# Kernel tuning notes

Hardware: AMD Instinct MI355X
Metric: run time of the kernel (lower is better)

Reference implementation:

```python
import jax, jax.numpy as jnp
import numpy as np

B, CIN, H, W = 8, 64, 128, 128
COUT, KH, KW = 64, 3, 3
STRIDE, PAD, DIL = 1, 1, 1
HO, WO = 128, 128


def setup_inputs() -> dict:
    key = jax.random.key(0)
    k1, k2, k3 = jax.random.split(key, 3)
    x = jax.random.normal(k1, (B, CIN, H, W), dtype=jnp.float32)
    offset = jax.random.normal(k2, (B, 2 * KH * KW, HO, WO), dtype=jnp.float32)
    fan_in = CIN * KH * KW
    weight = jax.random.normal(k3, (COUT, CIN, KH, KW), dtype=jnp.float32) / np.sqrt(fan_in)
    return {"x": x, "offset": offset, "weight": weight}


def _deform_conv(x, offset, weight):
    b, c, h, w = x.shape
    cout, cin, kh, kw = weight.shape
    k2 = kh * kw
    ho, wo = offset.shape[2], offset.shape[3]
    # offsets: interleaved (dy, dx) per kernel tap
    off = offset.reshape(b, k2, 2, ho, wo)
    dy, dx = off[:, :, 0], off[:, :, 1]                      # [B, K2, Ho, Wo]
    ky = jnp.repeat(jnp.arange(kh), kw).astype(x.dtype)       # [K2]
    kx = jnp.tile(jnp.arange(kw), kh).astype(x.dtype)
    base_y = (jnp.arange(ho) * STRIDE - PAD).astype(x.dtype)  # [Ho]
    base_x = (jnp.arange(wo) * STRIDE - PAD).astype(x.dtype)  # [Wo]
    py = dy + ky[None, :, None, None] * DIL + base_y[None, None, :, None]
    px = dx + kx[None, :, None, None] * DIL + base_x[None, None, None, :]

    y0 = jnp.floor(py)
    x0 = jnp.floor(px)
    wy1 = py - y0
    wx1 = px - x0
    y0i = y0.astype(jnp.int32)
    x0i = x0.astype(jnp.int32)

    def gather_corner(yi, xi, wgt):
        # zero-padding semantics: mask out-of-bounds corners
        valid = ((yi >= 0) & (yi < h) & (xi >= 0) & (xi < w)).astype(x.dtype)
        yc = jnp.clip(yi, 0, h - 1)
        xc = jnp.clip(xi, 0, w - 1)
        def per_batch(xb, yb, xbid, vb, wb):
            return xb[:, yb, xbid] * (vb * wb)[None]          # [C, K2, Ho, Wo]
        return jax.vmap(per_batch)(x, yc, xc, valid, wgt)

    # accumulate 4 corners to avoid holding all gathers at once
    sampled = gather_corner(y0i, x0i, (1 - wy1) * (1 - wx1))
    sampled = sampled + gather_corner(y0i, x0i + 1, (1 - wy1) * wx1)
    sampled = sampled + gather_corner(y0i + 1, x0i, wy1 * (1 - wx1))
    sampled = sampled + gather_corner(y0i + 1, x0i + 1, wy1 * wx1)
    # sampled: [B, Cin, K2, Ho, Wo]; conv-accumulate
    return jnp.einsum('bckhw,ock->bohw', sampled, weight.reshape(cout, cin, k2))


def reference(x, offset, weight):
    return _deform_conv(x, offset, weight)
```

## Files before the change

### kernel.cpp

```cpp
#include <hip/hip_runtime.h>
#include <hip/hip_bf16.h>

#define CIN  64
#define HH   128
#define WW   128
#define COUT 64
#define K2   9
#define HW   (HH * WW)

typedef __attribute__((ext_vector_type(8))) short bf16x8;
typedef __attribute__((ext_vector_type(4))) float f32x4;
typedef __attribute__((ext_vector_type(2))) float f32x2;

__device__ __forceinline__ unsigned short f2bf(float f) {
    __hip_bfloat16 h = __float2bfloat16(f);
    return *reinterpret_cast<unsigned short*>(&h);
}
__device__ __forceinline__ f32x2 up2(unsigned int d) {
    f32x2 r;
    r[0] = __uint_as_float(d << 16);
    r[1] = __uint_as_float(d & 0xffff0000u);
    return r;
}
__device__ __forceinline__ void gl2lds16(const unsigned short* g, unsigned short* l) {
    __builtin_amdgcn_global_load_lds(
        (const __attribute__((address_space(1))) unsigned int*)g,
        (__attribute__((address_space(3))) unsigned int*)l, 16, 0, 0);
}

__launch_bounds__(256)
__global__ void xprep2_kernel(const float* __restrict__ x, unsigned short* __restrict__ xt) {
    const int idx = blockIdx.x * 256 + threadIdx.x;
    const int xw = idx & 127;
    const int y  = (idx >> 7) & 127;
    const int s  = (idx >> 14) & 7;
    const int b  = idx >> 17;
    const float* src = x + (((size_t)(b * CIN + s * 8) * HH) + y) * WW + xw;
    union { unsigned short us[8]; bf16x8 v; } u;
    #pragma unroll
    for (int j = 0; j < 8; ++j) u.us[j] = f2bf(src[(size_t)j * HW]);
    *(bf16x8*)(xt + ((((size_t)b * 8 + s) * HW) + y * WW + xw) * 8) = u.v;
}

__global__ void wprep_kernel(const float* __restrict__ w, unsigned short* __restrict__ wtp) {
    int idx = blockIdx.x * 256 + threadIdx.x;
    if (idx >= COUT * CIN * K2) return;
    int j  = idx & 7;
    int l  = (idx >> 3) & 63;
    int nt = (idx >> 9) & 3;
    int ks = (idx >> 11) & 1;
    int k  = idx >> 12;
    int o  = nt * 16 + (l & 15);
    int c  = ks * 32 + (l >> 4) * 8 + j;
    wtp[idx] = f2bf(w[(o * CIN + c) * K2 + k]);
}

__launch_bounds__(512, 4)
__global__ void dcn_kernel(const unsigned short* __restrict__ xt,
                           const float* __restrict__ off,
                           const unsigned short* __restrict__ wtp,
                           float* __restrict__ out) {
    extern __shared__ unsigned short lsB[];
    const int tid = threadIdx.x;
    const int w   = tid >> 6;
    const int l   = tid & 63;
    const int wr  = w & 3;
    const int wh  = w >> 2;

    int bid = blockIdx.x;
    bid = (bid & 7) * 256 + (bid >> 3);
    const int b   = bid >> 8;
    const int t   = bid & 255;
    const int ty0 = (t >> 3) << 2;
    const int tx0 = (t & 7) << 4;

    const int g      = l >> 4;
    const int lane16 = l & 15;

    #pragma unroll
    for (int r = 0; r < 9; ++r) {
        const int seg = r * 8 + w;
        gl2lds16(wtp + seg * 512 + l * 8, lsB + seg * 512);
    }

    f32x4 acc[4] = {{0,0,0,0},{0,0,0,0},{0,0,0,0},{0,0,0,0}};

    const float* offb = off + (size_t)b * (2 * K2) * HW;
    const unsigned short* xp = xt + ((size_t)b * 8 + (wh * 4 + g)) * HW * 8;

    const int ypA  = ty0 + wr;
    const int xpA  = tx0 + lane16;
    const int offp = ypA * WW + xpA;

    f32x4 Pw[2];
    int   Pr0[2], Pr1[2];
    float oyv[2], oxv[2];
    bf16x8 Gst[2][4];
    bf16x8 bvv[4];
    bf16x8 af;

#define PARAMS(K, S) do {                                                     \
    const int kdy = (K) / 3 - 1, kdx = (K) % 3 - 1;                           \
    float py = oyv[S] + (float)(ypA + kdy);                                   \
    float px = oxv[S] + (float)(xpA + kdx);                                   \
    float fy = floorf(py), fx = floorf(px);                                   \
    float wy = py - fy, wxn = px - fx;                                        \
    int y0 = (int)fy, x0i = (int)fx;                                          \
    int yc0 = min(max(y0,     0), HH - 1);                                    \
    int yc1 = min(max(y0 + 1, 0), HH - 1);                                    \
    float ay0 = (y0 >= 0  && y0 <= HH - 1) ? (1.f - wy) : 0.f;                \
    float ay1 = (y0 >= -1 && y0 <= HH - 2) ? wy         : 0.f;                \
    int   xL  = min(max(x0i, 0), WW - 2);                                     \
    float bx0 = (x0i >= 0  && x0i <= WW - 1) ? (1.f - wxn) : 0.f;             \
    float bx1 = (x0i >= -1 && x0i <= WW - 2) ? wxn         : 0.f;             \
    bool  sw  = (x0i != xL);                                                  \
    float wxa = sw ? bx1 : bx0;                                               \
    float wxb = sw ? bx0 : bx1;                                               \
    Pw[S][0] = ay0 * wxa; Pw[S][1] = ay0 * wxb;                               \
    Pw[S][2] = ay1 * wxa; Pw[S][3] = ay1 * wxb;                               \
    Pr0[S] = (yc0 * WW + xL) * 8;                                             \
    Pr1[S] = (yc1 * WW + xL) * 8;                                             \
} while (0)

#define GATHER(S) do {                                                        \
    const unsigned short* r0p = xp + Pr0[S];                                  \
    const unsigned short* r1p = xp + Pr1[S];                                  \
    Gst[S][0] = *(const bf16x8*)(r0p); Gst[S][1] = *(const bf16x8*)(r0p + 8); \
    Gst[S][2] = *(const bf16x8*)(r1p); Gst[S][3] = *(const bf16x8*)(r1p + 8); \
} while (0)

#define INTERP(S) do {                                                        \
    union { bf16x8 v; unsigned int d[4]; } ua, ub, uc, ud;                    \
    ua.v = Gst[S][0]; ub.v = Gst[S][1]; uc.v = Gst[S][2]; ud.v = Gst[S][3];   \
    union { unsigned short us[8]; bf16x8 v; } rr;                             \
    _Pragma("unroll")                                                         \
    for (int q = 0; q < 4; ++q) {                                             \
        f32x2 v = up2(ua.d[q]) * Pw[S][0] + up2(ub.d[q]) * Pw[S][1]           \
                + up2(uc.d[q]) * Pw[S][2] + up2(ud.d[q]) * Pw[S][3];          \
        rr.us[2*q]   = f2bf(v[0]);                                            \
        rr.us[2*q+1] = f2bf(v[1]);                                            \
    }                                                                         \
    af = rr.v;                                                                \
} while (0)

#define BVLOAD(K) do {                                                        \
    _Pragma("unroll")                                                         \
    for (int nt = 0; nt < 4; ++nt)                                            \
        bvv[nt] = *(const bf16x8*)(&lsB[(((K) * 2 + wh) * 4 + nt) * 512 + l * 8]); \
} while (0)

#define DOMFMA() do {                                                         \
    __builtin_amdgcn_s_setprio(1);                                            \
    acc[0] = __builtin_amdgcn_mfma_f32_16x16x32_bf16(af, bvv[0], acc[0], 0, 0, 0); \
    acc[1] = __builtin_amdgcn_mfma_f32_16x16x32_bf16(af, bvv[1], acc[1], 0, 0, 0); \
    acc[2] = __builtin_amdgcn_mfma_f32_16x16x32_bf16(af, bvv[2], acc[2], 0, 0, 0); \
    acc[3] = __builtin_amdgcn_mfma_f32_16x16x32_bf16(af, bvv[3], acc[3], 0, 0, 0); \
    __builtin_amdgcn_s_setprio(0);                                            \
} while (0)

    oyv[0] = offb[offp];          oxv[0] = offb[HW + offp];
    oyv[1] = offb[2 * HW + offp]; oxv[1] = offb[3 * HW + offp];
    PARAMS(0, 0);
    GATHER(0);
    __syncthreads();

    #pragma unroll
    for (int s = 0; s < K2; ++s) {
        const int cur = s & 1, nxt = cur ^ 1;
        if (s < 8) {
            PARAMS(s + 1, nxt);
            if (s < 7) {
                oyv[cur] = offb[(2 * (s + 2)    ) * HW + offp];
                oxv[cur] = offb[(2 * (s + 2) + 1) * HW + offp];
            }
            GATHER(nxt);
        }
        BVLOAD(s);
        INTERP(cur);
        DOMFMA();
    }

#undef PARAMS
#undef GATHER
#undef INTERP
#undef BVLOAD
#undef DOMFMA

    float (*sred)[66] = (float (*)[66])lsB;
    __syncthreads();
    const int rq = g * 4;
    if (wh == 0) {
        #pragma unroll
        for (int nt = 0; nt < 4; ++nt)
            #pragma unroll
            for (int j = 0; j < 4; ++j)
                sred[wr * 16 + rq + j][nt * 16 + lane16] = acc[nt][j];
    }
    __syncthreads();
    if (wh == 1) {
        #pragma unroll
        for (int nt = 0; nt < 4; ++nt) {
            f32x4 v;
            #pragma unroll
            for (int j = 0; j < 4; ++j)
                v[j] = sred[wr * 16 + rq + j][nt * 16 + lane16] + acc[nt][j];
            const int o  = nt * 16 + lane16;
            const int yy = ty0 + wr;
            const int xx = tx0 + rq;
            *(f32x4*)&out[(((size_t)b * COUT + o) * HH + yy) * WW + xx] = v;
        }
    }
}

__global__ void wprep_fb(const float* __restrict__ w, unsigned short* __restrict__ wt) {
    int idx = blockIdx.x * 256 + threadIdx.x;
    if (idx >= COUT * CIN * K2) return;
    int o = idx / (CIN * K2);
    int r = idx % (CIN * K2);
    int k = r / CIN;
    int c = r % CIN;
    wt[idx] = f2bf(w[o * (CIN * K2) + c * K2 + k]);
}

__launch_bounds__(256)
__global__ void dcn_fb(const float* __restrict__ x, const float* __restrict__ off,
                       const unsigned short* __restrict__ wt, float* __restrict__ out) {
    __shared__ unsigned short s_s[64 * 66];
    const int tid = threadIdx.x;
    const int w = tid >> 6, l = tid & 63;
    const int bid = blockIdx.x;
    const int b = bid >> 8, t = bid & 255;
    const int ty0 = (t >> 4) << 3, tx0 = (t & 15) << 3;
    const int iy = l >> 3, ix = l & 7;
    const int ypix = ty0 + iy, xpix = tx0 + ix;
    f32x4 acc[4] = {{0,0,0,0},{0,0,0,0},{0,0,0,0},{0,0,0,0}};
    const int c0w = w * 16;
    for (int k = 0; k < K2; ++k) {
        float dy = off[(((b * (2*K2)) + 2*k    ) * HH + ypix) * WW + xpix];
        float dx = off[(((b * (2*K2)) + 2*k + 1) * HH + ypix) * WW + xpix];
        float py = dy + (float)(k / 3 + ypix - 1);
        float px = dx + (float)(k % 3 + xpix - 1);
        float fy = floorf(py), fx = floorf(px);
        float wy = py - fy, wx = px - fx;
        int y0 = (int)fy, x0 = (int)fx;
        int yc0 = min(max(y0, 0), HH-1), yc1 = min(max(y0+1, 0), HH-1);
        float ay0 = (y0 >= 0 && y0 <= HH-1) ? (1.f-wy) : 0.f;
        float ay1 = (y0 >= -1 && y0 <= HH-2) ? wy : 0.f;
        int xL = min(max(x0, 0), WW-2);
        float bx0 = (x0 >= 0 && x0 <= WW-1) ? (1.f-wx) : 0.f;
        float bx1 = (x0 >= -1 && x0 <= WW-2) ? wx : 0.f;
        bool sw = (x0 != xL);
        float wxa = sw ? bx1 : bx0, wxb = sw ? bx0 : bx1;
        float W0x = ay0*wxa, W0y = ay0*wxb, W1x = ay1*wxa, W1y = ay1*wxb;
        const float* r0 = x + ((b * CIN + c0w) * HH + yc0) * WW + xL;
        const float* r1 = x + ((b * CIN + c0w) * HH + yc1) * WW + xL;
        unsigned short* sd = &s_s[l * 66 + c0w];
        #pragma unroll
        for (int cc = 0; cc < 16; ++cc) {
            sd[cc] = f2bf(W0x*r0[0] + W0y*r0[1] + W1x*r1[0] + W1y*r1[1]);
            r0 += HH*WW; r1 += HH*WW;
        }
        __syncthreads();
        const int o_lane = l & 15, q = l >> 4;
        #pragma unroll
        for (int ks = 0; ks < 2; ++ks) {
            const int cb = ks*32 + q*8;
            const int row = w*16 + o_lane;
            const unsigned int* sp = (const unsigned int*)s_s;
            const int ib = row*33 + (cb >> 1);
            union { unsigned int u[4]; bf16x8 v; } af;
            af.u[0]=sp[ib]; af.u[1]=sp[ib+1]; af.u[2]=sp[ib+2]; af.u[3]=sp[ib+3];
            #pragma unroll
            for (int nt = 0; nt < 4; ++nt) {
                bf16x8 bfv = *(const bf16x8*)(wt + (nt*16 + o_lane) * (CIN*K2) + k*64 + cb);
                acc[nt] = __builtin_amdgcn_mfma_f32_16x16x32_bf16(af.v, bfv, acc[nt], 0, 0, 0);
            }
        }
        __syncthreads();
    }
    const int o_lane = l & 15, rq = (l >> 4) * 4;
    #pragma unroll
    for (int nt = 0; nt < 4; ++nt) {
        const int o = nt*16 + o_lane;
        #pragma unroll
        for (int j = 0; j < 4; ++j) {
            const int pix = w*16 + rq + j;
            out[(((size_t)b * COUT + o) * HH + ty0 + (pix>>3)) * WW + tx0 + (pix&7)] = acc[nt][j];
        }
    }
}

extern "C" void kernel_launch(void* const* d_in, const int* in_sizes, int n_in,
                              void* d_out, int out_size, void* d_ws, size_t ws_size,
                              hipStream_t stream) {
    const float* x   = (const float*)d_in[0];
    const float* off = (const float*)d_in[1];
    const float* wgt = (const float*)d_in[2];
    float* out = (float*)d_out;

    const size_t xt_bytes = (size_t)8 * HW * 64 * sizeof(unsigned short);
    const size_t wt_bytes = (size_t)COUT * CIN * K2 * sizeof(unsigned short);

    if (ws_size >= xt_bytes + wt_bytes) {
        unsigned short* xt  = (unsigned short*)d_ws;
        unsigned short* wtp = (unsigned short*)((char*)d_ws + xt_bytes);
        xprep2_kernel<<<4096, 256, 0, stream>>>(x, xt);
        wprep_kernel<<<(COUT * CIN * K2 + 255) / 256, 256, 0, stream>>>(wgt, wtp);
        dcn_kernel<<<2048, 512, 73728, stream>>>(xt, off, wtp, out);
    } else {
        unsigned short* wt = (unsigned short*)d_ws;
        wprep_fb<<<(COUT * CIN * K2 + 255) / 256, 256, 0, stream>>>(wgt, wt);
        dcn_fb<<<2048, 256, 0, stream>>>(x, off, wt, out);
    }
}
```

Measured before the change: 57.34 us.

## Deepen gather pipeline to triple buffering with offsets prefetched further ahead

Turns the double-buffered per-tap gather pipeline into a triple-buffered one. Corner gathers are now issued two kernel taps ahead of the MFMA step, and offset loads three taps ahead, using a hand-unrolled schedule of step macros. The goal is to hide more global-memory gather latency behind interpolation and MFMA work. In exchange it holds an extra set of bf16x8 gather registers and parameters, which raises register pressure and could cut occupancy.

Result: slower. 84.83 us (+47.9%).

```diff
diff --git a/kernel.cpp b/kernel.cpp
--- a/kernel.cpp
+++ b/kernel.cpp
@@ -92,17 +92,22 @@
     const int xpA  = tx0 + lane16;
     const int offp = ypA * WW + xpA;
 
-    f32x4 Pw[2];
-    int   Pr0[2], Pr1[2];
-    float oyv[2], oxv[2];
-    bf16x8 Gst[2][4];
+    f32x4 Pw[3];
+    int   Pr0[3], Pr1[3];
+    float oy[3], ox[3];
+    bf16x8 Gst[3][4];
     bf16x8 bvv[4];
     bf16x8 af;
 
+#define OFFL(K, S) do {                                                       \
+    oy[S] = offb[(2 * (K)    ) * HW + offp];                                  \
+    ox[S] = offb[(2 * (K) + 1) * HW + offp];                                  \
+} while (0)
+
 #define PARAMS(K, S) do {                                                     \
     const int kdy = (K) / 3 - 1, kdx = (K) % 3 - 1;                           \
-    float py = oyv[S] + (float)(ypA + kdy);                                   \
-    float px = oxv[S] + (float)(xpA + kdx);                                   \
+    float py = oy[S] + (float)(ypA + kdy);                                    \
+    float px = ox[S] + (float)(xpA + kdx);                                    \
     float fy = floorf(py), fx = floorf(px);                                   \
     float wy = py - fy, wxn = px - fx;                                        \
     int y0 = (int)fy, x0i = (int)fx;                                          \
@@ -158,33 +163,43 @@
     __builtin_amdgcn_s_setprio(0);                                            \
 } while (0)
 
-    oyv[0] = offb[offp];          oxv[0] = offb[HW + offp];
-    oyv[1] = offb[2 * HW + offp]; oxv[1] = offb[3 * HW + offp];
-    PARAMS(0, 0);
-    GATHER(0);
+#define STEPA(S, SC, SP, KO, SO) do {                                         \
+    PARAMS((S) + 2, SP); GATHER(SP); OFFL(KO, SO);                            \
+    BVLOAD(S); INTERP(SC); DOMFMA();                                          \
+} while (0)
+#define STEPB(S, SC, SP) do {                                                 \
+    PARAMS((S) + 2, SP); GATHER(SP);                                          \
+    BVLOAD(S); INTERP(SC); DOMFMA();                                          \
+} while (0)
+#define STEPC(S, SC) do {                                                     \
+    BVLOAD(S); INTERP(SC); DOMFMA();                                          \
+} while (0)
+
+    OFFL(0, 0); OFFL(1, 1); OFFL(2, 2);
+    PARAMS(0, 0); GATHER(0);
+    OFFL(3, 0);
+    PARAMS(1, 1); GATHER(1);
     __syncthreads();
 
-    #pragma unroll
-    for (int s = 0; s < K2; ++s) {
-        const int cur = s & 1, nxt = cur ^ 1;
-        if (s < 8) {
-            PARAMS(s + 1, nxt);
-            if (s < 7) {
-                oyv[cur] = offb[(2 * (s + 2)    ) * HW + offp];
-                oxv[cur] = offb[(2 * (s + 2) + 1) * HW + offp];
-            }
-            GATHER(nxt);
-        }
-        BVLOAD(s);
-        INTERP(cur);
-        DOMFMA();
-    }
-
+    STEPA(0, 0, 2, 4, 1);
+    STEPA(1, 1, 0, 5, 2);
+    STEPA(2, 2, 1, 6, 0);
+    STEPA(3, 0, 2, 7, 1);
+    STEPA(4, 1, 0, 8, 2);
+    STEPB(5, 2, 1);
+    STEPB(6, 0, 2);
+    STEPC(7, 1);
+    STEPC(8, 2);
+
+#undef OFFL
 #undef PARAMS
 #undef GATHER
 #undef INTERP
 #undef BVLOAD
 #undef DOMFMA
+#undef STEPA
+#undef STEPB
+#undef STEPC
 
     float (*sred)[66] = (float (*)[66])lsB;
     __syncthreads();
```
